# Kernel tuning notes

Hardware: AMD Instinct MI355X
Metric: run time of the kernel (lower is better)

The kernel has to match this reference:

```python
import jax, jax.numpy as jnp
import numpy as np

N, D_IN = 40000, 3000
E = 640000
ALPHA = 0.9
BN_EPS = 0.001      # nn.BatchNorm in encoder/decoder blocks (eps=0.001)
BN_EPS_CONV = 1e-5  # PyG BatchNorm default eps
NEG_SLOPE = 0.2     # GATConv leaky_relu slope


def _bn(x, g, b, m, v, eps):
    # inference-mode batchnorm with running stats
    return (x - m) * (g / jnp.sqrt(v + eps)) + b


def _gat(h, src, dst, W, a_src, a_dst, bias, n):
    # PyG GATConv (heads=1): linear transform, per-edge additive attention,
    # segment softmax over incoming edges (self-loops already in src/dst).
    hw = h @ W                                   # [n, out]
    s_src = (hw * a_src).sum(-1)                 # [n]
    s_dst = (hw * a_dst).sum(-1)                 # [n]
    al = jax.nn.leaky_relu(s_src[src] + s_dst[dst], NEG_SLOPE)  # [e]
    mx = jax.ops.segment_max(al, dst, num_segments=n)
    e = jnp.exp(al - mx[dst])
    z = jax.ops.segment_sum(e, dst, num_segments=n)
    w = e / (z[dst] + 1e-16)                     # softmax weight per edge
    out = jax.ops.segment_sum(w[:, None] * hw[src], dst, num_segments=n)
    return out + bias


def _forward(x, edge_index,
             e0_w, e0_b, e0_g, e0_beta, e0_m, e0_v,
             e1_w, e1_b, e1_g, e1_beta, e1_m, e1_v,
             g1_w, g1_as, g1_ad, g1_b, bnc_g, bnc_beta, bnc_m, bnc_v,
             gm_w, gm_as, gm_ad, gm_b,
             gv_w, gv_as, gv_ad, gv_b,
             d0_w, d0_b, d0_g, d0_beta, d0_m, d0_v,
             out_w, out_b, cluster, eps):
    ar = jnp.arange(N, dtype=edge_index.dtype)
    src = jnp.concatenate([edge_index[0], ar])   # add self-loops (GATConv default)
    dst = jnp.concatenate([edge_index[1], ar])

    # linear encoder: Linear -> BN -> ELU (dropout inactive at eval)
    h = jax.nn.elu(_bn(x @ e0_w + e0_b, e0_g, e0_beta, e0_m, e0_v, BN_EPS))
    feat_x = jax.nn.elu(_bn(h @ e1_w + e1_b, e1_g, e1_beta, e1_m, e1_v, BN_EPS))

    # graph conv stack
    c = _gat(feat_x, src, dst, g1_w, g1_as, g1_ad, g1_b, N)
    c = jax.nn.relu(_bn(c, bnc_g, bnc_beta, bnc_m, bnc_v, BN_EPS_CONV))
    mu = _gat(c, src, dst, gm_w, gm_as, gm_ad, gm_b, N)
    logvar = _gat(c, src, dst, gv_w, gv_as, gv_ad, gv_b, N)

    # reparameterize (std = exp(logvar) per original code)
    gnn_z = eps * jnp.exp(logvar) + mu
    z = jnp.concatenate([feat_x, gnn_z], axis=1)  # [N, 28]

    # linear decoder
    d = jax.nn.elu(_bn(z @ d0_w + d0_b, d0_g, d0_beta, d0_m, d0_v, BN_EPS))
    de_feat = d @ out_w + out_b                   # [N, D_IN]

    # DEC student-t soft assignment (squared distance via expansion)
    sq = jnp.maximum(
        jnp.sum(z * z, 1)[:, None] + jnp.sum(cluster * cluster, 1)[None, :]
        - 2.0 * (z @ cluster.T), 0.0)             # [N, K]
    q = 1.0 / (1.0 + sq / ALPHA + 1e-8)
    q = q ** ((ALPHA + 1.0) / 2.0)
    q = q / jnp.sum(q, 1, keepdims=True)
    return z, mu, logvar, de_feat, q, feat_x, gnn_z


def setup_inputs() -> dict:
    key = jax.random.key(0)
    ks = iter(jax.random.split(key, 48))
    nrm = lambda shape, s=0.1: jax.random.normal(next(ks), shape, jnp.float32) * s
    pos = lambda shape: jax.random.uniform(next(ks), shape, jnp.float32, 0.5, 1.5)
    inp = {}
    inp['x'] = jax.random.normal(next(ks), (N, D_IN), jnp.float32)
    inp['edge_index'] = jax.random.randint(next(ks), (2, E), 0, N, jnp.int32)
    # encoder L0: 3000 -> 32
    inp.update(e0_w=nrm((D_IN, 32), 0.02), e0_b=nrm((32,)), e0_g=pos((32,)),
               e0_beta=nrm((32,)), e0_m=nrm((32,)), e0_v=pos((32,)))
    # encoder L1: 32 -> 20
    inp.update(e1_w=nrm((32, 20)), e1_b=nrm((20,)), e1_g=pos((20,)),
               e1_beta=nrm((20,)), e1_m=nrm((20,)), e1_v=pos((20,)))
    # GATConv 20 -> 64 (+ PyG BatchNorm)
    inp.update(g1_w=nrm((20, 64)), g1_as=nrm((64,)), g1_ad=nrm((64,)), g1_b=nrm((64,)),
               bnc_g=pos((64,)), bnc_beta=nrm((64,)), bnc_m=nrm((64,)), bnc_v=pos((64,)))
    # GATConv mean / logvar: 64 -> 8
    inp.update(gm_w=nrm((64, 8)), gm_as=nrm((8,)), gm_ad=nrm((8,)), gm_b=nrm((8,)))
    inp.update(gv_w=nrm((64, 8)), gv_as=nrm((8,)), gv_ad=nrm((8,)), gv_b=nrm((8,)))
    # decoder L0: 28 -> 32, out: 32 -> 3000
    inp.update(d0_w=nrm((28, 32)), d0_b=nrm((32,)), d0_g=pos((32,)),
               d0_beta=nrm((32,)), d0_m=nrm((32,)), d0_v=pos((32,)))
    inp.update(out_w=nrm((32, D_IN), 0.05), out_b=nrm((D_IN,)))
    inp['cluster'] = nrm((15, 28), 0.5)
    inp['eps'] = jax.random.normal(next(ks), (N, 8), jnp.float32)
    return inp


def reference(x, edge_index,
              e0_w, e0_b, e0_g, e0_beta, e0_m, e0_v,
              e1_w, e1_b, e1_g, e1_beta, e1_m, e1_v,
              g1_w, g1_as, g1_ad, g1_b, bnc_g, bnc_beta, bnc_m, bnc_v,
              gm_w, gm_as, gm_ad, gm_b,
              gv_w, gv_as, gv_ad, gv_b,
              d0_w, d0_b, d0_g, d0_beta, d0_m, d0_v,
              out_w, out_b, cluster, eps):
    return _forward(x, edge_index,
                    e0_w, e0_b, e0_g, e0_beta, e0_m, e0_v,
                    e1_w, e1_b, e1_g, e1_beta, e1_m, e1_v,
                    g1_w, g1_as, g1_ad, g1_b, bnc_g, bnc_beta, bnc_m, bnc_v,
                    gm_w, gm_as, gm_ad, gm_b,
                    gv_w, gv_as, gv_ad, gv_b,
                    d0_w, d0_b, d0_g, d0_beta, d0_m, d0_v,
                    out_w, out_b, cluster, eps)
```

## Files before the change

kernel.cpp:

```cpp
#include <hip/hip_runtime.h>
#include <cfloat>
#include <cmath>

#define NN 40000
#define DIN 3000
#define NE 640000
#define ET (NE + NN)

#define NKS 94
#define NKH 47
#define NCT 192
#define NB_E 2657

typedef __attribute__((ext_vector_type(8))) short short8;
typedef __attribute__((ext_vector_type(4))) float f32x4;

union frag16 { short8 s; uint4 u; };

__device__ __forceinline__ float lrelu(float x) { return x >= 0.f ? x : 0.2f * x; }
__device__ __forceinline__ float elu(float x)   { return x > 0.f ? x : expm1f(x); }
__device__ __forceinline__ unsigned f2bf(float f) {
    unsigned u = __float_as_uint(f);
    return (u + 0x7FFFu + ((u >> 16) & 1u)) >> 16;
}
__device__ __forceinline__ float bf2f(unsigned short us) {
    return __uint_as_float((unsigned)us << 16);
}

__global__ void k_deg_prep(const int* __restrict__ ei, int* __restrict__ deg,
                           const float* __restrict__ w, const float* __restrict__ ow,
                           unsigned short* __restrict__ bfw,
                           unsigned short* __restrict__ bfragb)
{
    if (blockIdx.x < NB_E) {
        int e = blockIdx.x * 256 + threadIdx.x;
        if (e >= ET) return;
        int d = (e < NE) ? ei[NE + e] : e - NE;
        atomicAdd(&deg[d], 1);
    } else {
        int id = (blockIdx.x - NB_E) * 256 + threadIdx.x;
        if (id < 96 * 128) {
            int ks = id >> 7, r = id & 127;
            int t = r >> 6, l = r & 63;
            int col = t * 16 + (l & 15);
            int k0 = ks * 32 + ((l >> 4) << 3);
            unsigned v[8];
            #pragma unroll
            for (int j = 0; j < 8; j++) {
                int k = k0 + j;
                v[j] = (k < DIN) ? f2bf(w[(size_t)k * 32 + col]) : 0u;
            }
            uint4 p;
            p.x = v[0] | (v[1] << 16); p.y = v[2] | (v[3] << 16);
            p.z = v[4] | (v[5] << 16); p.w = v[6] | (v[7] << 16);
            *(uint4*)&bfw[(size_t)id * 8] = p;
        } else {
            int tt = id - 96 * 128;
            if (tt < NCT * 64) {
                int ct = tt >> 6, l = tt & 63;
                int col = ct * 16 + (l & 15);
                int k0 = (l >> 4) * 8;
                uint4 p = make_uint4(0u, 0u, 0u, 0u);
                if (col < DIN) {
                    unsigned v[8];
                    #pragma unroll
                    for (int j = 0; j < 8; j++)
                        v[j] = f2bf(ow[(size_t)(k0 + j) * DIN + col]);
                    p.x = v[0] | (v[1] << 16); p.y = v[2] | (v[3] << 16);
                    p.z = v[4] | (v[5] << 16); p.w = v[6] | (v[7] << 16);
                }
                *(uint4*)&bfragb[((size_t)ct * 64 + l) * 8] = p;
            }
        }
    }
}

__global__ __launch_bounds__(1024) void k_scan(const int* __restrict__ deg,
                                               int* __restrict__ start) {
    __shared__ int sums[1024];
    const int t = threadIdx.x;
    const int base = t * 40;
    int4 buf[10];
    #pragma unroll
    for (int i = 0; i < 10; i++) buf[i] = ((const int4*)(deg + base))[i];
    int s = 0;
    #pragma unroll
    for (int i = 0; i < 10; i++) {
        int b0 = base + i * 4;
        if (b0 + 0 < NN) s += buf[i].x;
        if (b0 + 1 < NN) s += buf[i].y;
        if (b0 + 2 < NN) s += buf[i].z;
        if (b0 + 3 < NN) s += buf[i].w;
    }
    sums[t] = s; __syncthreads();
    for (int off = 1; off < 1024; off <<= 1) {
        int v = sums[t];
        int add = (t >= off) ? sums[t - off] : 0;
        __syncthreads();
        sums[t] = v + add;
        __syncthreads();
    }
    int run = (t > 0) ? sums[t - 1] : 0;
    #pragma unroll
    for (int i = 0; i < 10; i++) {
        int b0 = base + i * 4;
        if (b0 + 0 < NN) { start[b0 + 0] = run; run += buf[i].x; }
        if (b0 + 1 < NN) { start[b0 + 1] = run; run += buf[i].y; }
        if (b0 + 2 < NN) { start[b0 + 2] = run; run += buf[i].z; }
        if (b0 + 3 < NN) { start[b0 + 3] = run; run += buf[i].w; }
    }
}

__global__ void k_fill(const int* __restrict__ ei, const int* __restrict__ start,
                       int* __restrict__ cnt, int* __restrict__ srcs) {
    int e = blockIdx.x * 256 + threadIdx.x;
    if (e >= ET) return;
    int s, d;
    if (e < NE) { s = ei[e]; d = ei[NE + e]; } else { s = d = e - NE; }
    int pos = start[d] + atomicAdd(&cnt[d], 1);
    srcs[pos] = s;
}

__global__ __launch_bounds__(128) void k_enc0(
    const float* __restrict__ x, const unsigned short* __restrict__ bfw,
    const float* __restrict__ b, const float* __restrict__ g,
    const float* __restrict__ beta, const float* __restrict__ m,
    const float* __restrict__ v, float* __restrict__ h)
{
    __shared__ float red[64 * 8];
    const int tid = threadIdx.x, wid = tid >> 6, l = tid & 63;
    const int gg = blockIdx.x;
    const int row = gg * 16 + (l & 15);
    const int klane = (l >> 4) << 3;

    const float* xp = x + (size_t)row * DIN + klane;
    const unsigned short* bp = bfw + (size_t)l * 8;

    f32x4 acc0 = {0.f, 0.f, 0.f, 0.f};
    f32x4 acc1 = {0.f, 0.f, 0.f, 0.f};

    const int ks0 = wid * NKH;
    #pragma unroll 2
    for (int ks = ks0; ks < ks0 + NKH; ks++) {
        frag16 a; a.u = make_uint4(0u, 0u, 0u, 0u);
        int k = ks * 32 + klane;
        if (k < DIN) {
            float4 v0 = *(const float4*)(xp + ks * 32);
            float4 v1 = *(const float4*)(xp + ks * 32 + 4);
            a.u.x = f2bf(v0.x) | (f2bf(v0.y) << 16);
            a.u.y = f2bf(v0.z) | (f2bf(v0.w) << 16);
            a.u.z = f2bf(v1.x) | (f2bf(v1.y) << 16);
            a.u.w = f2bf(v1.z) | (f2bf(v1.w) << 16);
        }
        frag16 b0, b1;
        b0.u = *(const uint4*)(bp + (size_t)(ks * 2 + 0) * 512);
        b1.u = *(const uint4*)(bp + (size_t)(ks * 2 + 1) * 512);
        acc0 = __builtin_amdgcn_mfma_f32_16x16x32_bf16(a.s, b0.s, acc0, 0, 0, 0);
        acc1 = __builtin_amdgcn_mfma_f32_16x16x32_bf16(a.s, b1.s, acc1, 0, 0, 0);
    }

    if (wid == 1) {
        #pragma unroll
        for (int r = 0; r < 4; r++) {
            red[l * 8 + r]     = acc0[r];
            red[l * 8 + 4 + r] = acc1[r];
        }
    }
    __syncthreads();
    if (wid != 0) return;
    #pragma unroll
    for (int r = 0; r < 4; r++) {
        acc0[r] += red[l * 8 + r];
        acc1[r] += red[l * 8 + 4 + r];
    }

    const int cl = l & 15;
    const int rbase = gg * 16 + (l >> 4) * 4;
    float sc0 = g[cl] * rsqrtf(v[cl] + 1e-3f);
    float sh0 = beta[cl] - m[cl] * sc0;
    float bb0 = b[cl];
    float sc1 = g[cl + 16] * rsqrtf(v[cl + 16] + 1e-3f);
    float sh1 = beta[cl + 16] - m[cl + 16] * sc1;
    float bb1 = b[cl + 16];
    #pragma unroll
    for (int reg = 0; reg < 4; reg++) {
        size_t o = (size_t)(rbase + reg) * 32;
        h[o + cl]      = elu((acc0[reg] + bb0) * sc0 + sh0);
        h[o + 16 + cl] = elu((acc1[reg] + bb1) * sc1 + sh1);
    }
}

__global__ void k_enc_prep(
    const float* __restrict__ h,
    const float* __restrict__ e1w, const float* __restrict__ e1b,
    const float* __restrict__ e1g, const float* __restrict__ e1beta,
    const float* __restrict__ e1m, const float* __restrict__ e1v,
    const float* __restrict__ g1w, const float* __restrict__ g1as,
    const float* __restrict__ g1ad,
    float* __restrict__ out_fx, unsigned short* __restrict__ hw1b,
    float* __restrict__ s1src, float* __restrict__ s1dst)
{
    int row = blockIdx.x * 256 + threadIdx.x;
    if (row >= NN) return;
    float hr[32];
    #pragma unroll
    for (int c4 = 0; c4 < 8; c4++) {
        float4 p = *(const float4*)&h[(size_t)row * 32 + c4 * 4];
        hr[c4 * 4 + 0] = p.x; hr[c4 * 4 + 1] = p.y;
        hr[c4 * 4 + 2] = p.z; hr[c4 * 4 + 3] = p.w;
    }
    float fx[20];
    #pragma unroll
    for (int c = 0; c < 20; c++) {
        float s = e1b[c];
        for (int k = 0; k < 32; k++) s += hr[k] * e1w[k * 20 + c];
        float sc = e1g[c] * rsqrtf(e1v[c] + 1e-3f);
        s = (s - e1m[c]) * sc + e1beta[c];
        fx[c] = elu(s);
        out_fx[(size_t)row * 20 + c] = fx[c];
    }
    float ss = 0.f, sd = 0.f;
    for (int c = 0; c < 64; c++) {
        float s = 0.f;
        for (int k = 0; k < 20; k++) s += fx[k] * g1w[k * 64 + c];
        hw1b[(size_t)row * 64 + c] = (unsigned short)f2bf(s);
        ss += s * g1as[c];
        sd += s * g1ad[c];
    }
    s1src[row] = ss; s1dst[row] = sd;
}

__global__ __launch_bounds__(256) void k_gat1_fused(
    const int* __restrict__ start, const int* __restrict__ deg,
    const int* __restrict__ srcs,
    const float* __restrict__ s1src, const float* __restrict__ s1dst,
    const unsigned short* __restrict__ hw1b,
    const float* __restrict__ g1b,
    const float* __restrict__ bncg, const float* __restrict__ bncbeta,
    const float* __restrict__ bncm, const float* __restrict__ bncv,
    const float* __restrict__ gmw, const float* __restrict__ gmas, const float* __restrict__ gmad,
    const float* __restrict__ gvw, const float* __restrict__ gvas, const float* __restrict__ gvad,
    float* __restrict__ hwm, float* __restrict__ hwv,
    float* __restrict__ smsrc, float* __restrict__ smdst,
    float* __restrict__ svsrc, float* __restrict__ svdst)
{
    __shared__ float cs[4][64];
    const int wv = threadIdx.x >> 6;
    int d = (blockIdx.x * 256 + threadIdx.x) >> 6;
    int l = threadIdx.x & 63;
    if (d >= NN) return;
    int j0 = start[d], n = deg[d];
    float sd = s1dst[d];
    float acc = 0.f, z = 0.f;
    int j = 0;
    for (; j + 4 <= n; j += 4) {
        int s0 = srcs[j0 + j], s1 = srcs[j0 + j + 1];
        int s2 = srcs[j0 + j + 2], s3 = srcs[j0 + j + 3];
        float a0 = s1src[s0], a1 = s1src[s1], a2 = s1src[s2], a3 = s1src[s3];
        float h0 = bf2f(hw1b[(size_t)s0 * 64 + l]);
        float h1 = bf2f(hw1b[(size_t)s1 * 64 + l]);
        float h2 = bf2f(hw1b[(size_t)s2 * 64 + l]);
        float h3 = bf2f(hw1b[(size_t)s3 * 64 + l]);
        float e0 = expf(lrelu(a0 + sd)), e1 = expf(lrelu(a1 + sd));
        float e2 = expf(lrelu(a2 + sd)), e3 = expf(lrelu(a3 + sd));
        z += (e0 + e1) + (e2 + e3);
        acc += e0 * h0; acc += e1 * h1; acc += e2 * h2; acc += e3 * h3;
    }
    for (; j < n; j++) {
        int s = srcs[j0 + j];
        float ex = expf(lrelu(s1src[s] + sd));
        z += ex;
        acc += ex * bf2f(hw1b[(size_t)s * 64 + l]);
    }
    float zi = 1.f / (z + 1e-16f);
    float val = acc * zi + g1b[l];
    float sc = bncg[l] * rsqrtf(bncv[l] + 1e-5f);
    val = (val - bncm[l]) * sc + bncbeta[l];
    float c = val > 0.f ? val : 0.f;
    cs[wv][l] = c;

    if (l < 16) {
        const bool isv = l >= 8;
        const int o = l & 7;
        const float* wmat = isv ? gvw : gmw;
        float s = 0.f;
        #pragma unroll 8
        for (int k = 0; k < 64; k++)
            s += cs[wv][k] * wmat[k * 8 + o];
        if (!isv) hwm[(size_t)d * 8 + o] = s;
        else      hwv[(size_t)d * 8 + o] = s;
        float u1 = s * (isv ? gvas[o] : gmas[o]);
        float u2 = s * (isv ? gvad[o] : gmad[o]);
        u1 += __shfl_xor(u1, 1); u1 += __shfl_xor(u1, 2); u1 += __shfl_xor(u1, 4);
        u2 += __shfl_xor(u2, 1); u2 += __shfl_xor(u2, 2); u2 += __shfl_xor(u2, 4);
        if (o == 0) {
            if (!isv) { smsrc[d] = u1; smdst[d] = u2; }
            else      { svsrc[d] = u1; svdst[d] = u2; }
        }
    }
}

__global__ __launch_bounds__(256) void k_gat23_gather(
    const int* __restrict__ start, const int* __restrict__ deg,
    const int* __restrict__ srcs,
    const float* __restrict__ smsrc, const float* __restrict__ smdst,
    const float* __restrict__ svsrc, const float* __restrict__ svdst,
    const float* __restrict__ hwm, const float* __restrict__ hwv,
    float* __restrict__ zm, float* __restrict__ accm,
    float* __restrict__ zv, float* __restrict__ accv)
{
    int d = (blockIdx.x * 256 + threadIdx.x) >> 6;
    int l = threadIdx.x & 63;
    if (d >= NN) return;
    const int eg = l >> 4;
    const bool isv = (l & 15) >= 8;
    const int f = l & 7;
    int j0 = start[d], n = deg[d];
    float sdst = isv ? svdst[d] : smdst[d];
    float acc = 0.f, z = 0.f;
    for (int j = eg; j < n; j += 4) {
        int s = srcs[j0 + j];
        float a = (isv ? svsrc[s] : smsrc[s]) + sdst;
        float ex = expf(lrelu(a));
        z += ex;
        float hv = isv ? hwv[(size_t)s * 8 + f] : hwm[(size_t)s * 8 + f];
        acc += ex * hv;
    }
    acc += __shfl_xor(acc, 16); acc += __shfl_xor(acc, 32);
    z   += __shfl_xor(z, 16);   z   += __shfl_xor(z, 32);
    if (l < 16) {
        if (!isv) { accm[(size_t)d * 8 + f] = acc; if (f == 0) zm[d] = z; }
        else      { accv[(size_t)d * 8 + f] = acc; if (f == 0) zv[d] = z; }
    }
}

__global__ void k_final(
    const float* __restrict__ accm, const float* __restrict__ zm, const float* __restrict__ gmb,
    const float* __restrict__ accv, const float* __restrict__ zv, const float* __restrict__ gvb,
    const float* __restrict__ epsin, const float* __restrict__ fx_out,
    const float* __restrict__ d0w, const float* __restrict__ d0b,
    const float* __restrict__ d0g, const float* __restrict__ d0beta,
    const float* __restrict__ d0m, const float* __restrict__ d0v,
    const float* __restrict__ cluster,
    float* __restrict__ out_z, float* __restrict__ out_mu, float* __restrict__ out_lv,
    float* __restrict__ out_q, float* __restrict__ out_gz,
    unsigned short* __restrict__ abuf)
{
    int row = blockIdx.x * 256 + threadIdx.x;
    if (row >= NN) return;
    float zvec[28];
    #pragma unroll
    for (int k = 0; k < 20; k++) zvec[k] = fx_out[(size_t)row * 20 + k];
    float zim = 1.f / (zm[row] + 1e-16f);
    float ziv = 1.f / (zv[row] + 1e-16f);
    #pragma unroll
    for (int o = 0; o < 8; o++) {
        float mu = accm[(size_t)row * 8 + o] * zim + gmb[o];
        float lv = accv[(size_t)row * 8 + o] * ziv + gvb[o];
        float gz = epsin[(size_t)row * 8 + o] * expf(lv) + mu;
        out_mu[(size_t)row * 8 + o] = mu;
        out_lv[(size_t)row * 8 + o] = lv;
        out_gz[(size_t)row * 8 + o] = gz;
        zvec[20 + o] = gz;
    }
    #pragma unroll
    for (int k = 0; k < 28; k++) out_z[(size_t)row * 28 + k] = zvec[k];
    float dv[32];
    #pragma unroll
    for (int c = 0; c < 32; c++) {
        float s = d0b[c];
        #pragma unroll
        for (int k = 0; k < 28; k++) s += zvec[k] * d0w[k * 32 + c];
        float sc = d0g[c] * rsqrtf(d0v[c] + 1e-3f);
        s = (s - d0m[c]) * sc + d0beta[c];
        dv[c] = elu(s);
    }
    int g = row >> 4, rl = row & 15;
    #pragma unroll
    for (int hh = 0; hh < 4; hh++) {
        uint4 p;
        p.x = f2bf(dv[hh*8+0]) | (f2bf(dv[hh*8+1]) << 16);
        p.y = f2bf(dv[hh*8+2]) | (f2bf(dv[hh*8+3]) << 16);
        p.z = f2bf(dv[hh*8+4]) | (f2bf(dv[hh*8+5]) << 16);
        p.w = f2bf(dv[hh*8+6]) | (f2bf(dv[hh*8+7]) << 16);
        *(uint4*)&abuf[(size_t)g * 512 + (rl + 16 * hh) * 8] = p;
    }
    float zz = 0.f;
    #pragma unroll
    for (int k = 0; k < 28; k++) zz += zvec[k] * zvec[k];
    float qv[15], qs = 0.f;
    for (int j = 0; j < 15; j++) {
        float cc = 0.f, zc = 0.f;
        for (int k = 0; k < 28; k++) {
            float cv = cluster[j * 28 + k];
            cc += cv * cv; zc += zvec[k] * cv;
        }
        float sq = zz + cc - 2.f * zc;
        if (sq < 0.f) sq = 0.f;
        float qb = 1.f / (1.f + sq * (1.f / 0.9f) + 1e-8f);
        qb = powf(qb, 0.95f);
        qv[j] = qb; qs += qb;
    }
    float qi = 1.f / qs;
    #pragma unroll
    for (int j = 0; j < 15; j++) out_q[(size_t)row * 15 + j] = qv[j] * qi;
}

#define OTS 132
__global__ __launch_bounds__(256) void k_dec_out(
    const unsigned short* __restrict__ abuf, const unsigned short* __restrict__ bfragb,
    const float* __restrict__ ob, float* __restrict__ out_de)
{
    __shared__ float ot[64 * OTS];
    const int tid = threadIdx.x, wid = tid >> 6, l = tid & 63;
    const int gblk = blockIdx.y;
    const int ct0 = blockIdx.x * 8;
    frag16 a; a.u = *(const uint4*)&abuf[((size_t)(gblk * 4 + wid)) * 512 + l * 8];
    const int lrow = wid * 16 + (l >> 4) * 4;
    const int cl = l & 15;
    #pragma unroll
    for (int c = 0; c < 8; c++) {
        frag16 bfr; bfr.u = *(const uint4*)&bfragb[((size_t)(ct0 + c) * 64 + l) * 8];
        f32x4 acc = {0.f, 0.f, 0.f, 0.f};
        acc = __builtin_amdgcn_mfma_f32_16x16x32_bf16(a.s, bfr.s, acc, 0, 0, 0);
        #pragma unroll
        for (int reg = 0; reg < 4; reg++)
            ot[(lrow + reg) * OTS + c * 16 + cl] = acc[reg];
    }
    __syncthreads();
    const int row0 = gblk * 64;
    const int c0 = ct0 * 16;
    #pragma unroll
    for (int i = 0; i < 8; i++) {
        int idx = i * 256 + tid;
        int r = idx >> 5, q = idx & 31;
        int col = c0 + q * 4;
        if (col < DIN) {
            const float* p = &ot[r * OTS + q * 4];
            float4 bq = *(const float4*)&ob[col];
            f32x4 o;
            o[0] = p[0] + bq.x; o[1] = p[1] + bq.y;
            o[2] = p[2] + bq.z; o[3] = p[3] + bq.w;
            __builtin_nontemporal_store(o, (f32x4*)&out_de[(size_t)(row0 + r) * DIN + col]);
        }
    }
}

extern "C" void kernel_launch(void* const* d_in, const int* in_sizes, int n_in,
                              void* d_out, int out_size, void* d_ws, size_t ws_size,
                              hipStream_t stream) {
    const float* x      = (const float*)d_in[0];
    const int*   ei     = (const int*)  d_in[1];
    const float* e0_w   = (const float*)d_in[2];
    const float* e0_b   = (const float*)d_in[3];
    const float* e0_g   = (const float*)d_in[4];
    const float* e0_be  = (const float*)d_in[5];
    const float* e0_m   = (const float*)d_in[6];
    const float* e0_v   = (const float*)d_in[7];
    const float* e1_w   = (const float*)d_in[8];
    const float* e1_b   = (const float*)d_in[9];
    const float* e1_g   = (const float*)d_in[10];
    const float* e1_be  = (const float*)d_in[11];
    const float* e1_m   = (const float*)d_in[12];
    const float* e1_v   = (const float*)d_in[13];
    const float* g1_w   = (const float*)d_in[14];
    const float* g1_as  = (const float*)d_in[15];
    const float* g1_ad  = (const float*)d_in[16];
    const float* g1_b   = (const float*)d_in[17];
    const float* bnc_g  = (const float*)d_in[18];
    const float* bnc_be = (const float*)d_in[19];
    const float* bnc_m  = (const float*)d_in[20];
    const float* bnc_v  = (const float*)d_in[21];
    const float* gm_w   = (const float*)d_in[22];
    const float* gm_as  = (const float*)d_in[23];
    const float* gm_ad  = (const float*)d_in[24];
    const float* gm_b   = (const float*)d_in[25];
    const float* gv_w   = (const float*)d_in[26];
    const float* gv_as  = (const float*)d_in[27];
    const float* gv_ad  = (const float*)d_in[28];
    const float* gv_b   = (const float*)d_in[29];
    const float* d0_w   = (const float*)d_in[30];
    const float* d0_b   = (const float*)d_in[31];
    const float* d0_g   = (const float*)d_in[32];
    const float* d0_be  = (const float*)d_in[33];
    const float* d0_m   = (const float*)d_in[34];
    const float* d0_v   = (const float*)d_in[35];
    const float* out_w  = (const float*)d_in[36];
    const float* out_b  = (const float*)d_in[37];
    const float* cluster= (const float*)d_in[38];
    const float* epsin  = (const float*)d_in[39];

    float* out = (float*)d_out;
    float* out_z  = out;
    float* out_mu = out + (size_t)NN * 28;
    float* out_lv = out + (size_t)NN * 36;
    float* out_de = out + (size_t)NN * 44;
    float* out_q  = out + (size_t)NN * 44 + (size_t)NN * DIN;
    float* out_fx = out + (size_t)NN * 59 + (size_t)NN * DIN;
    float* out_gz = out + (size_t)NN * 79 + (size_t)NN * DIN;

    float* ws = (float*)d_ws;
    const size_t n = NN;
    float* hbuf = ws;
    unsigned short* hw1b = (unsigned short*)(ws + 64 * n);
    float* s1src   = ws + 96 * n;
    float* s1dst   = ws + 97 * n;
    unsigned short* abuf   = (unsigned short*)(ws + 103 * n);
    unsigned short* bfw    = (unsigned short*)(ws + 119 * n);
    unsigned short* bfragb = (unsigned short*)(ws + 121 * n);
    float* hwm   = ws;
    float* hwv   = ws + 8 * n;
    float* smsrc = ws + 16 * n;
    float* smdst = ws + 17 * n;
    float* svsrc = ws + 18 * n;
    float* svdst = ws + 19 * n;
    float* zm    = ws + 20 * n;
    float* zv    = ws + 21 * n;
    float* accm  = ws + 22 * n;
    float* accv  = ws + 30 * n;

    int* srcs  = (int*)out_de;
    int* deg   = srcs + ET;
    int* cnt   = deg + NN;
    int* start = cnt + NN;

    const int NB_ROWS = (NN + 255) / 256;
    const int NB_PREP = (96 * 128 + NCT * 64 + 255) / 256;

    (void)hipMemsetAsync(deg, 0, 2 * NN * sizeof(int), stream);
    k_deg_prep<<<NB_E + NB_PREP, 256, 0, stream>>>(ei, deg, e0_w, out_w, bfw, bfragb);
    k_scan<<<1, 1024, 0, stream>>>(deg, start);
    k_fill<<<NB_E, 256, 0, stream>>>(ei, start, cnt, srcs);

    k_enc0<<<NN / 16, 128, 0, stream>>>(x, bfw, e0_b, e0_g, e0_be, e0_m, e0_v, hbuf);
    k_enc_prep<<<NB_ROWS, 256, 0, stream>>>(hbuf, e1_w, e1_b, e1_g, e1_be, e1_m, e1_v,
                                            g1_w, g1_as, g1_ad,
                                            out_fx, hw1b, s1src, s1dst);
    k_gat1_fused<<<(NN * 64 + 255) / 256, 256, 0, stream>>>(start, deg, srcs,
                                                            s1src, s1dst, hw1b,
                                                            g1_b, bnc_g, bnc_be, bnc_m, bnc_v,
                                                            gm_w, gm_as, gm_ad,
                                                            gv_w, gv_as, gv_ad,
                                                            hwm, hwv, smsrc, smdst, svsrc, svdst);
    k_gat23_gather<<<(NN * 64 + 255) / 256, 256, 0, stream>>>(start, deg, srcs,
                                                              smsrc, smdst, svsrc, svdst,
                                                              hwm, hwv, zm, accm, zv, accv);
    k_final<<<NB_ROWS, 256, 0, stream>>>(accm, zm, gm_b, accv, zv, gv_b, epsin, out_fx,
                                         d0_w, d0_b, d0_g, d0_be, d0_m, d0_v, cluster,
                                         out_z, out_mu, out_lv, out_q, out_gz, abuf);
    dim3 dec_grid(NCT / 8, NN / 64);
    k_dec_out<<<dec_grid, 256, 0, stream>>>(abuf, bfragb, out_b, out_de);
}
```

Baseline: 508.2 us.

## Fuse CSR fill into encoder prep and final epilogue into GAT gather

The CSR edge-fill kernel is merged into the encoder-prep kernel as extra blocks, so both run in one launch. The final per-row epilogue (mu/logvar, reparameterization, decoder layer 0, cluster soft-assignment, bf16 packing) is moved into the GAT2/3 gather kernel. It now works per wavefront with shared memory and shuffles instead of one thread per row. This removes two launches and the round trip of the acc/z intermediates through global memory. In exchange, the epilogue runs on few lanes per wavefront, and the fused fill blocks compete with the prep work.

```diff
diff --git a/kernel.cpp b/kernel.cpp
--- a/kernel.cpp
+++ b/kernel.cpp
@@ -11,6 +11,7 @@
 #define NKH 47
 #define NCT 192
 #define NB_E 2657
+#define NB_ROWS 157
 
 typedef __attribute__((ext_vector_type(8))) short short8;
 typedef __attribute__((ext_vector_type(4))) float f32x4;
@@ -111,16 +112,6 @@
     }
 }
 
-__global__ void k_fill(const int* __restrict__ ei, const int* __restrict__ start,
-                       int* __restrict__ cnt, int* __restrict__ srcs) {
-    int e = blockIdx.x * 256 + threadIdx.x;
-    if (e >= ET) return;
-    int s, d;
-    if (e < NE) { s = ei[e]; d = ei[NE + e]; } else { s = d = e - NE; }
-    int pos = start[d] + atomicAdd(&cnt[d], 1);
-    srcs[pos] = s;
-}
-
 __global__ __launch_bounds__(128) void k_enc0(
     const float* __restrict__ x, const unsigned short* __restrict__ bfw,
     const float* __restrict__ b, const float* __restrict__ g,
@@ -190,7 +181,7 @@
     }
 }
 
-__global__ void k_enc_prep(
+__global__ void k_prep_fill(
     const float* __restrict__ h,
     const float* __restrict__ e1w, const float* __restrict__ e1b,
     const float* __restrict__ e1g, const float* __restrict__ e1beta,
@@ -198,8 +189,20 @@
     const float* __restrict__ g1w, const float* __restrict__ g1as,
     const float* __restrict__ g1ad,
     float* __restrict__ out_fx, unsigned short* __restrict__ hw1b,
-    float* __restrict__ s1src, float* __restrict__ s1dst)
+    float* __restrict__ s1src, float* __restrict__ s1dst,
+    const int* __restrict__ ei, const int* __restrict__ start,
+    int* __restrict__ cnt, int* __restrict__ srcs)
 {
+    if (blockIdx.x >= NB_ROWS) {
+        int e = (blockIdx.x - NB_ROWS) * 256 + threadIdx.x;
+        if (e < ET) {
+            int s, d;
+            if (e < NE) { s = ei[e]; d = ei[NE + e]; } else { s = d = e - NE; }
+            int pos = start[d] + atomicAdd(&cnt[d], 1);
+            srcs[pos] = s;
+        }
+        return;
+    }
     int row = blockIdx.x * 256 + threadIdx.x;
     if (row >= NN) return;
     float hr[32];
@@ -300,15 +303,25 @@
     }
 }
 
-__global__ __launch_bounds__(256) void k_gat23_gather(
+__global__ __launch_bounds__(256) void k_gat23_final(
     const int* __restrict__ start, const int* __restrict__ deg,
     const int* __restrict__ srcs,
     const float* __restrict__ smsrc, const float* __restrict__ smdst,
     const float* __restrict__ svsrc, const float* __restrict__ svdst,
     const float* __restrict__ hwm, const float* __restrict__ hwv,
-    float* __restrict__ zm, float* __restrict__ accm,
-    float* __restrict__ zv, float* __restrict__ accv)
+    const float* __restrict__ gmb, const float* __restrict__ gvb,
+    const float* __restrict__ epsin, const float* __restrict__ fx_out,
+    const float* __restrict__ d0w, const float* __restrict__ d0b,
+    const float* __restrict__ d0g, const float* __restrict__ d0beta,
+    const float* __restrict__ d0m, const float* __restrict__ d0v,
+    const float* __restrict__ cluster,
+    float* __restrict__ out_z, float* __restrict__ out_mu, float* __restrict__ out_lv,
+    float* __restrict__ out_q, float* __restrict__ out_gz,
+    unsigned short* __restrict__ abuf)
 {
+    __shared__ float zs[4][28];
+    __shared__ float dvs[4][32];
+    const int wv = threadIdx.x >> 6;
     int d = (blockIdx.x * 256 + threadIdx.x) >> 6;
     int l = threadIdx.x & 63;
     if (d >= NN) return;
@@ -328,82 +341,54 @@
     }
     acc += __shfl_xor(acc, 16); acc += __shfl_xor(acc, 32);
     z   += __shfl_xor(z, 16);   z   += __shfl_xor(z, 32);
-    if (l < 16) {
-        if (!isv) { accm[(size_t)d * 8 + f] = acc; if (f == 0) zm[d] = z; }
-        else      { accv[(size_t)d * 8 + f] = acc; if (f == 0) zv[d] = z; }
-    }
-}
-
-__global__ void k_final(
-    const float* __restrict__ accm, const float* __restrict__ zm, const float* __restrict__ gmb,
-    const float* __restrict__ accv, const float* __restrict__ zv, const float* __restrict__ gvb,
-    const float* __restrict__ epsin, const float* __restrict__ fx_out,
-    const float* __restrict__ d0w, const float* __restrict__ d0b,
-    const float* __restrict__ d0g, const float* __restrict__ d0beta,
-    const float* __restrict__ d0m, const float* __restrict__ d0v,
-    const float* __restrict__ cluster,
-    float* __restrict__ out_z, float* __restrict__ out_mu, float* __restrict__ out_lv,
-    float* __restrict__ out_q, float* __restrict__ out_gz,
-    unsigned short* __restrict__ abuf)
-{
-    int row = blockIdx.x * 256 + threadIdx.x;
-    if (row >= NN) return;
-    float zvec[28];
-    #pragma unroll
-    for (int k = 0; k < 20; k++) zvec[k] = fx_out[(size_t)row * 20 + k];
-    float zim = 1.f / (zm[row] + 1e-16f);
-    float ziv = 1.f / (zv[row] + 1e-16f);
-    #pragma unroll
-    for (int o = 0; o < 8; o++) {
-        float mu = accm[(size_t)row * 8 + o] * zim + gmb[o];
-        float lv = accv[(size_t)row * 8 + o] * ziv + gvb[o];
-        float gz = epsin[(size_t)row * 8 + o] * expf(lv) + mu;
-        out_mu[(size_t)row * 8 + o] = mu;
-        out_lv[(size_t)row * 8 + o] = lv;
-        out_gz[(size_t)row * 8 + o] = gz;
-        zvec[20 + o] = gz;
-    }
-    #pragma unroll
-    for (int k = 0; k < 28; k++) out_z[(size_t)row * 28 + k] = zvec[k];
-    float dv[32];
-    #pragma unroll
-    for (int c = 0; c < 32; c++) {
-        float s = d0b[c];
+    float zi = 1.f / (z + 1e-16f);
+    float t = acc * zi + (isv ? gvb[f] : gmb[f]);
+    float partner = __shfl_xor(t, 8);
+    float gz = 0.f;
+    if (l < 8) gz = epsin[(size_t)d * 8 + f] * expf(partner) + t;
+    if (l < 8)        { out_mu[(size_t)d * 8 + f] = t; out_gz[(size_t)d * 8 + f] = gz; }
+    else if (l < 16)  { out_lv[(size_t)d * 8 + f] = t; }
+    if (l < 20) zs[wv][l] = fx_out[(size_t)d * 20 + l];
+    if (l < 8)  zs[wv][20 + l] = gz;
+    if (l < 28) out_z[(size_t)d * 28 + l] = zs[wv][l];
+    if (l < 32) {
+        float s = d0b[l];
         #pragma unroll
-        for (int k = 0; k < 28; k++) s += zvec[k] * d0w[k * 32 + c];
-        float sc = d0g[c] * rsqrtf(d0v[c] + 1e-3f);
-        s = (s - d0m[c]) * sc + d0beta[c];
-        dv[c] = elu(s);
-    }
-    int g = row >> 4, rl = row & 15;
-    #pragma unroll
-    for (int hh = 0; hh < 4; hh++) {
+        for (int k = 0; k < 28; k++) s += zs[wv][k] * d0w[k * 32 + l];
+        float sc = d0g[l] * rsqrtf(d0v[l] + 1e-3f);
+        s = (s - d0m[l]) * sc + d0beta[l];
+        dvs[wv][l] = elu(s);
+    }
+    if (l < 4) {
+        int g = d >> 4, rl = d & 15;
+        const float* dv = dvs[wv];
         uint4 p;
-        p.x = f2bf(dv[hh*8+0]) | (f2bf(dv[hh*8+1]) << 16);
-        p.y = f2bf(dv[hh*8+2]) | (f2bf(dv[hh*8+3]) << 16);
-        p.z = f2bf(dv[hh*8+4]) | (f2bf(dv[hh*8+5]) << 16);
-        p.w = f2bf(dv[hh*8+6]) | (f2bf(dv[hh*8+7]) << 16);
-        *(uint4*)&abuf[(size_t)g * 512 + (rl + 16 * hh) * 8] = p;
+        p.x = f2bf(dv[l*8+0]) | (f2bf(dv[l*8+1]) << 16);
+        p.y = f2bf(dv[l*8+2]) | (f2bf(dv[l*8+3]) << 16);
+        p.z = f2bf(dv[l*8+4]) | (f2bf(dv[l*8+5]) << 16);
+        p.w = f2bf(dv[l*8+6]) | (f2bf(dv[l*8+7]) << 16);
+        *(uint4*)&abuf[(size_t)g * 512 + (rl + 16 * l) * 8] = p;
     }
     float zz = 0.f;
     #pragma unroll
-    for (int k = 0; k < 28; k++) zz += zvec[k] * zvec[k];
-    float qv[15], qs = 0.f;
-    for (int j = 0; j < 15; j++) {
+    for (int k = 0; k < 28; k++) { float zk = zs[wv][k]; zz += zk * zk; }
+    float qb = 0.f;
+    if (l < 15) {
         float cc = 0.f, zc = 0.f;
+        #pragma unroll
         for (int k = 0; k < 28; k++) {
-            float cv = cluster[j * 28 + k];
-            cc += cv * cv; zc += zvec[k] * cv;
+            float cv = cluster[l * 28 + k];
+            cc += cv * cv; zc += zs[wv][k] * cv;
         }
         float sq = zz + cc - 2.f * zc;
         if (sq < 0.f) sq = 0.f;
-        float qb = 1.f / (1.f + sq * (1.f / 0.9f) + 1e-8f);
+        qb = 1.f / (1.f + sq * (1.f / 0.9f) + 1e-8f);
         qb = powf(qb, 0.95f);
-        qv[j] = qb; qs += qb;
-    }
-    float qi = 1.f / qs;
-    #pragma unroll
-    for (int j = 0; j < 15; j++) out_q[(size_t)row * 15 + j] = qv[j] * qi;
+    }
+    float qs = qb;
+    qs += __shfl_xor(qs, 1); qs += __shfl_xor(qs, 2);
+    qs += __shfl_xor(qs, 4); qs += __shfl_xor(qs, 8);
+    if (l < 15) out_q[(size_t)d * 15 + l] = qb / qs;
 }
 
 #define OTS 132
@@ -514,40 +499,36 @@
     float* smdst = ws + 17 * n;
     float* svsrc = ws + 18 * n;
     float* svdst = ws + 19 * n;
-    float* zm    = ws + 20 * n;
-    float* zv    = ws + 21 * n;
-    float* accm  = ws + 22 * n;
-    float* accv  = ws + 30 * n;
 
     int* srcs  = (int*)out_de;
     int* deg   = srcs + ET;
     int* cnt   = deg + NN;
     int* start = cnt + NN;
 
-    const int NB_ROWS = (NN + 255) / 256;
     const int NB_PREP = (96 * 128 + NCT * 64 + 255) / 256;
 
     (void)hipMemsetAsync(deg, 0, 2 * NN * sizeof(int), stream);
     k_deg_prep<<<NB_E + NB_PREP, 256, 0, stream>>>(ei, deg, e0_w, out_w, bfw, bfragb);
     k_scan<<<1, 1024, 0, stream>>>(deg, start);
-    k_fill<<<NB_E, 256, 0, stream>>>(ei, start, cnt, srcs);
 
     k_enc0<<<NN / 16, 128, 0, stream>>>(x, bfw, e0_b, e0_g, e0_be, e0_m, e0_v, hbuf);
-    k_enc_prep<<<NB_ROWS, 256, 0, stream>>>(hbuf, e1_w, e1_b, e1_g, e1_be, e1_m, e1_v,
-                                            g1_w, g1_as, g1_ad,
-                                            out_fx, hw1b, s1src, s1dst);
+    k_prep_fill<<<NB_ROWS + NB_E, 256, 0, stream>>>(hbuf, e1_w, e1_b, e1_g, e1_be, e1_m, e1_v,
+                                                    g1_w, g1_as, g1_ad,
+                                                    out_fx, hw1b, s1src, s1dst,
+                                                    ei, start, cnt, srcs);
     k_gat1_fused<<<(NN * 64 + 255) / 256, 256, 0, stream>>>(start, deg, srcs,
                                                             s1src, s1dst, hw1b,
                                                             g1_b, bnc_g, bnc_be, bnc_m, bnc_v,
                                                             gm_w, gm_as, gm_ad,
                                                             gv_w, gv_as, gv_ad,
                                                             hwm, hwv, smsrc, smdst, svsrc, svdst);
-    k_gat23_gather<<<(NN * 64 + 255) / 256, 256, 0, stream>>>(start, deg, srcs,
-                                                              smsrc, smdst, svsrc, svdst,
-                                                              hwm, hwv, zm, accm, zv, accv);
-    k_final<<<NB_ROWS, 256, 0, stream>>>(accm, zm, gm_b, accv, zv, gv_b, epsin, out_fx,
-                                         d0_w, d0_b, d0_g, d0_be, d0_m, d0_v, cluster,
-                                         out_z, out_mu, out_lv, out_q, out_gz, abuf);
+    k_gat23_final<<<(NN * 64 + 255) / 256, 256, 0, stream>>>(start, deg, srcs,
+                                                             smsrc, smdst, svsrc, svdst,
+                                                             hwm, hwv, gm_b, gv_b, epsin, out_fx,
+                                                             d0_w, d0_b, d0_g, d0_be, d0_m, d0_v,
+                                                             cluster,
+                                                             out_z, out_mu, out_lv, out_q, out_gz,
+                                                             abuf);
     dim3 dec_grid(NCT / 8, NN / 64);
     k_dec_out<<<dec_grid, 256, 0, stream>>>(abuf, bfragb, out_b, out_de);
 }
```

New measurement: 484.3 us. 1.05x faster.
